# Kernel tuning notes

Hardware: AMD Instinct MI355X
Metric: run time of the kernel (lower is better)

The kernel has to match this reference:

```python
import jax, jax.numpy as jnp
import numpy as np

NPOINT = 1024
NSAMPLE = 32
RADIUS = 0.2


def index_points2(points, idx):
    # points: (B,N,D), idx: (B,S) -> (B,S,D)
    return jnp.take_along_axis(points, idx[..., None], axis=1)


def index_points3(points, idx):
    # points: (B,N,D), idx: (B,S,K) -> (B,S,K,D)
    B, S, K = idx.shape
    flat = jnp.take_along_axis(points, idx.reshape(B, S * K)[..., None], axis=1)
    return flat.reshape(B, S, K, points.shape[-1])


def farthest_point_sampling(xyz, npoint):
    # xyz: (B,N,3) -> (B,npoint) int32 indices. First point deterministic (index 0).
    B, N, _ = xyz.shape
    first = jnp.zeros((B,), jnp.int32)
    chosen = jnp.zeros((B, npoint), jnp.int32).at[:, 0].set(first)
    first_xyz = index_points2(xyz, first[:, None])[:, 0, :]
    dist_min = jnp.sum((xyz - first_xyz[:, None, :]) ** 2, axis=-1)  # (B,N)

    def body(i, carry):
        chosen, dist_min = carry
        far = jnp.argmax(dist_min, axis=-1).astype(jnp.int32)  # (B,)
        far_xyz = index_points2(xyz, far[:, None])[:, 0, :]
        d = jnp.sum((xyz - far_xyz[:, None, :]) ** 2, axis=-1)
        return chosen.at[:, i].set(far), jnp.minimum(dist_min, d)

    chosen, _ = jax.lax.fori_loop(1, npoint, body, (chosen, dist_min))
    return chosen


def query_ball_point(radius, nsample, xyz, new_xyz):
    # (B,S,N) squared distances; out-of-ball -> inf; take nsample nearest (stable argsort).
    dist = jnp.sum((new_xyz[:, :, None, :] - xyz[:, None, :, :]) ** 2, axis=-1)
    dist_m = jnp.where(dist <= radius ** 2, dist, jnp.inf)
    return jnp.argsort(dist_m, axis=-1)[:, :, :nsample]


def mlp2(x, Wa, ba, Wb, bb, act2):
    h = jax.nn.relu(x @ Wa + ba)
    return act2(h @ Wb + bb)


def reference(xyz, features, W1, b1, W2, b2, W3, b3, W4, b4):
    fps_idx = farthest_point_sampling(xyz, NPOINT)          # (B,S)
    new_xyz = index_points2(xyz, fps_idx)                   # (B,S,3)
    group_idx = query_ball_point(RADIUS, NSAMPLE, xyz, new_xyz)  # (B,S,K)
    grouped_xyz = index_points3(xyz, group_idx)             # (B,S,K,3)
    grouped_xyz_norm = grouped_xyz - new_xyz[:, :, None, :]
    grouped_feats = index_points3(features, group_idx)      # (B,S,K,C)
    f_in = jnp.concatenate([grouped_xyz_norm, grouped_feats], axis=-1)
    f_prime = mlp2(f_in, W1, b1, W2, b2, jax.nn.relu)       # (B,S,K,H)
    f_mean = jnp.mean(f_prime, axis=2, keepdims=True)
    w_in = jnp.concatenate([grouped_xyz_norm, f_prime - f_mean], axis=-1)
    alpha = mlp2(w_in, W3, b3, W4, b4, jax.nn.sigmoid)      # (B,S,K,H)
    f_out = jnp.sum(alpha * f_prime, axis=2)                # (B,S,H)
    return new_xyz, f_out


def setup_inputs() -> dict:
    key = jax.random.key(0)
    ks = jax.random.split(key, 8)
    B, N, C, H = 16, 4096, 64, 128
    xyz = jax.random.uniform(ks[0], (B, N, 3), dtype=jnp.float32)
    features = jax.random.normal(ks[1], (B, N, C), dtype=jnp.float32)
    s = 0.1
    return {
        "xyz": xyz,
        "features": features,
        "W1": jax.random.normal(ks[2], (3 + C, H), dtype=jnp.float32) * s,
        "b1": jnp.zeros((H,), jnp.float32),
        "W2": jax.random.normal(ks[3], (H, H), dtype=jnp.float32) * s,
        "b2": jnp.zeros((H,), jnp.float32),
        "W3": jax.random.normal(ks[4], (3 + H, H), dtype=jnp.float32) * s,
        "b3": jnp.zeros((H,), jnp.float32),
        "W4": jax.random.normal(ks[5], (H, H), dtype=jnp.float32) * s,
        "b4": jnp.zeros((H,), jnp.float32),
    }
```

## Files before the change

### kernel.cpp

```cpp
#include <hip/hip_runtime.h>

typedef unsigned short u16;
typedef unsigned int   u32;
typedef unsigned long long u64;
typedef short s8v __attribute__((ext_vector_type(8)));
typedef float f4v __attribute__((ext_vector_type(4)));
typedef float f2v __attribute__((ext_vector_type(2)));

#define STRIDE 168
#define CAP 512
#define OFF_G1 0
#define OFF_G2 12288
#define OFF_G3 28672
#define OFF_G4 49152

__device__ __forceinline__ float bf2f(u16 u){ return __uint_as_float(((u32)u)<<16); }
__device__ __forceinline__ u16 f2bf(float f){
  u32 u = __float_as_uint(f);
  return (u16)((u + 0x7FFFu + ((u>>16)&1u)) >> 16);
}
__device__ __forceinline__ float sqd(float ax,float ay,float az,float bx,float by,float bz){
  float dx=ax-bx, dy=ay-by, dz=az-bz;
  return __fadd_rn(__fadd_rn(__fmul_rn(dx,dx),__fmul_rn(dy,dy)),__fmul_rn(dz,dz));
}

#define WMAX_STEP(v, CTRL) { \
  u32 _t = (u32)__builtin_amdgcn_update_dpp(0, (int)(v), CTRL, 0xf, 0xf, false); \
  (v) = (v) > _t ? (v) : _t; }
#define QMAX64(k, CTRL) { \
  u32 _lo=(u32)(k), _hi=(u32)((k)>>32); \
  u32 _plo=(u32)__builtin_amdgcn_update_dpp(0,(int)_lo,CTRL,0xf,0xf,true); \
  u32 _phi=(u32)__builtin_amdgcn_update_dpp(0,(int)_hi,CTRL,0xf,0xf,true); \
  u64 _o=((u64)_phi<<32)|_plo; (k) = (k)>_o ? (k) : _o; }

__global__ __launch_bounds__(256) void fps_kernel(const float* __restrict__ xyz,
                                                  float* __restrict__ newxyz){
  __shared__ __align__(16) float S[4096*3];
  __shared__ u64 red[2][4];
  const int b = blockIdx.x, tid = threadIdx.x;
  const int lane = tid & 63, wv = tid >> 6;
  const float* xb = xyz + (size_t)b*4096*3;
  #pragma unroll
  for(int j=0;j<12;j++) ((float4*)S)[j*256+tid] = ((const float4*)xb)[j*256+tid];
  __syncthreads();
  f2v X[8],Y[8],Z[8],DM[8];
  const float x0=S[0], y0=S[1], z0=S[2];
  {
    #pragma clang fp contract(off)
    const f2v fx2={x0,x0}, fy2={y0,y0}, fz2={z0,z0};
    #pragma unroll
    for(int k2=0;k2<8;k2++){
      int p0 = tid*16 + 2*k2;
      X[k2] = (f2v){S[p0*3],   S[p0*3+3]};
      Y[k2] = (f2v){S[p0*3+1], S[p0*3+4]};
      Z[k2] = (f2v){S[p0*3+2], S[p0*3+5]};
      f2v dx=X[k2]-fx2, dy=Y[k2]-fy2, dz=Z[k2]-fz2;
      DM[k2] = (dx*dx + dy*dy) + dz*dz;
    }
  }
  if(tid==0){
    size_t o=(size_t)b*1024*3;
    newxyz[o]=x0; newxyz[o+1]=y0; newxyz[o+2]=z0;
  }
  for(int i=1;i<1024;i++){
    float vm = DM[0][0]; int jm = 0;
    #pragma unroll
    for(int j=1;j<16;j++){
      float dj = DM[j>>1][j&1];
      bool g = dj > vm; vm = g ? dj : vm; jm = g ? j : jm;
    }
    u32 w = __float_as_uint(vm);
    WMAX_STEP(w, 0x111); WMAX_STEP(w, 0x112); WMAX_STEP(w, 0x114);
    WMAX_STEP(w, 0x118); WMAX_STEP(w, 0x142); WMAX_STEP(w, 0x143);
    u32 wm = (u32)__builtin_amdgcn_readlane((int)w, 63);
    u64 msk = __ballot(__float_as_uint(vm) == wm);
    int ldr = __ffsll((unsigned long long)msk) - 1;
    int pj  = __builtin_amdgcn_readlane(jm, ldr);
    int p   = (wv*64 + ldr)*16 + pj;
    if(lane==0) red[i&1][wv] = ((u64)wm<<32) | (u32)(~(u32)p);
    __syncthreads();
    u64 k = red[i&1][lane&3];
    QMAX64(k, 0xB1); QMAX64(k, 0x4E);
    int far = (int)(~(u32)k) & 4095;
    float fx=S[far*3], fy=S[far*3+1], fz=S[far*3+2];
    if(tid==0){
      size_t o=((size_t)b*1024+i)*3;
      newxyz[o]=fx; newxyz[o+1]=fy; newxyz[o+2]=fz;
    }
    {
      #pragma clang fp contract(off)
      const f2v fx2={fx,fx}, fy2={fy,fy}, fz2={fz,fz};
      #pragma unroll
      for(int k2=0;k2<8;k2++){
        f2v dx=X[k2]-fx2, dy=Y[k2]-fy2, dz=Z[k2]-fz2;
        f2v s = (dx*dx + dy*dy) + dz*dz;
        DM[k2] = __builtin_elementwise_min(DM[k2], s);
      }
    }
  }
}

__global__ __launch_bounds__(256) void swz_kernel(const float* __restrict__ W1,const float* __restrict__ W2,
                                                  const float* __restrict__ W3,const float* __restrict__ W4,
                                                  u16* __restrict__ wsw){
  int T = blockIdx.x*256 + threadIdx.x;
  const float* W; int rel, base, kind;
  if(T < 1536){ rel=T;      base=OFF_G1; W=W1; kind=0; }
  else if(T < 3584){ rel=T-1536; base=OFF_G2; W=W2; kind=1; }
  else if(T < 6144){ rel=T-3584; base=OFF_G3; W=W3; kind=0; }
  else         { rel=T-6144; base=OFF_G4; W=W4; kind=1; }
  int chunk=rel>>6, lane=rel&63, c=chunk>>3, t=chunk&7, quad=lane>>4, l15=lane&15;
  u16 v[8];
  #pragma unroll
  for(int j=0;j<8;j++){
    int kp = c*32 + quad*8 + j, n = t*16 + l15;
    int src = (kind==0) ? (kp<3 ? kp : (kp>=32 ? kp-29 : -1)) : kp;
    v[j] = (src<0) ? (u16)0 : f2bf(W[src*128 + n]);
  }
  int4 o;
  o.x=(int)((u32)v[0]|((u32)v[1]<<16)); o.y=(int)((u32)v[2]|((u32)v[3]<<16));
  o.z=(int)((u32)v[4]|((u32)v[5]<<16)); o.w=(int)((u32)v[6]|((u32)v[7]<<16));
  *(int4*)&wsw[base + rel*8] = o;
}

__device__ __forceinline__ void zero_C(f4v C[2][8]){
  #pragma unroll
  for(int mt=0;mt<2;mt++)
    #pragma unroll
    for(int t=0;t<8;t++) C[mt][t] = (f4v){0.f,0.f,0.f,0.f};
}
__device__ __forceinline__ void load_bias(const float* bsrc,int l15,float bb[8]){
  #pragma unroll
  for(int t=0;t<8;t++) bb[t]=bsrc[t*16+l15];
}
template<int KC>
__device__ __forceinline__ void run_gemm(const u16* A, const u16* BW,
                                         int lane,int l15,int quad, f4v C[2][8]){
  s8v af[2][KC];
  #pragma unroll
  for(int mt=0;mt<2;mt++)
    #pragma unroll
    for(int c=0;c<KC;c++)
      af[mt][c] = *(const s8v*)&A[(mt*16+l15)*STRIDE + c*32 + quad*8];
  #pragma unroll
  for(int t=0;t<8;t++){
    #pragma unroll
    for(int c=0;c<KC;c++){
      s8v bw = *(const s8v*)&BW[((c*8+t)*64 + lane)*8];
      C[0][t] = __builtin_amdgcn_mfma_f32_16x16x32_bf16(af[0][c],bw,C[0][t],0,0,0);
      C[1][t] = __builtin_amdgcn_mfma_f32_16x16x32_bf16(af[1][c],bw,C[1][t],0,0,0);
    }
  }
}
__device__ __forceinline__ void store_act(u16* A,int l15,int quad,f4v C[2][8],const float bb[8]){
  #pragma unroll
  for(int mt=0;mt<2;mt++)
    #pragma unroll
    for(int t=0;t<8;t++)
      #pragma unroll
      for(int r=0;r<4;r++){
        float v = fmaxf(C[mt][t][r]+bb[t], 0.f);
        A[(mt*16+quad*4+r)*STRIDE + t*16 + l15] = f2bf(v);
      }
}
__device__ __forceinline__ void write_xyz_chunk0(u16* A,int lane,float xn,float yn,float zn){
  if(lane<32){
    u16* row=&A[lane*STRIDE];
    row[0]=f2bf(xn); row[1]=f2bf(yn); row[2]=f2bf(zn); row[3]=0;
    #pragma unroll
    for(int q=0;q<7;q++) *(u64*)&row[4+q*4] = 0ull;
  }
}

__global__ __launch_bounds__(256,2) void mlp_kernel(const float* __restrict__ xyz,
    const float* __restrict__ feats, const u16* __restrict__ wsw,
    const float* __restrict__ b1,const float* __restrict__ b2,const float* __restrict__ b3,const float* __restrict__ b4,
    const float* __restrict__ newxyz, float* __restrict__ fout){
  __shared__ __align__(16) u16 Abuf[4][32*STRIDE];
  __shared__ u64 Bcand[4][CAP];
  __shared__ int selbuf[4][32];
  const int tid=threadIdx.x, wv=tid>>6, lane=tid&63, quad=lane>>4, l15=lane&15;
  const int widx = blockIdx.x*4 + wv, b = widx>>10;
  u16* A = Abuf[wv];
  const float* xb = xyz + (size_t)b*4096*3;
  const float cx=newxyz[widx*3], cy=newxyz[widx*3+1], cz=newxyz[widx*3+2];

  {
    u64* Bc = Bcand[wv];
    int* sel = selbuf[wv];
    const u64 lt = (1ull<<lane)-1ull;
    int base=0;
    for(int kk=0;kk<64;kk++){
      int p = kk*64 + lane;
      float d = sqd(cx,cy,cz, xb[p*3],xb[p*3+1],xb[p*3+2]);
      bool in = (d <= 0.04f);
      u64 m = __ballot(in);
      if(in){ int pos = base + __popcll(m&lt); if(pos<CAP) Bc[pos] = ((u64)__float_as_uint(d)<<32)|(u32)p; }
      base += __popcll(m);
    }
    int cnt = base>CAP ? CAP : base;
    if(cnt > 32){
      for(int c=lane; c<cnt; c+=64){
        u64 key = Bc[c]; int r=0;
        for(int t2=0;t2<cnt;t2++) r += (Bc[t2] < key) ? 1 : 0;
        if(r < 32) sel[r] = (int)(u32)key;
      }
    } else {
      for(int c=lane; c<cnt; c+=64) sel[c] = (int)(u32)Bc[c];
      int need = 32 - cnt, b2 = 0;
      for(int kk=0; kk<64 && b2<need; kk++){
        int p = kk*64 + lane;
        float d = sqd(cx,cy,cz, xb[p*3],xb[p*3+1],xb[p*3+2]);
        bool o = !(d <= 0.04f);
        u64 m = __ballot(o);
        if(o){ int pos = b2 + __popcll(m&lt); if(pos<need) sel[cnt+pos] = p; }
        b2 += __popcll(m);
      }
    }
  }
  const int* sel = selbuf[wv];
  const int gi_f = sel[lane>>1] & 4095;
  const int gi_x = sel[lane & 31] & 4095;

  {
    int r2=lane>>1, h=lane&1;
    const float* fs = feats + ((size_t)b*4096 + gi_f)*64 + h*32;
    u16* fd = &A[r2*STRIDE + 32 + h*32];
    #pragma unroll
    for(int j=0;j<8;j++){
      float4 v4 = ((const float4*)fs)[j];
      u64 pk4 = (u64)f2bf(v4.x) | ((u64)f2bf(v4.y)<<16)
              | ((u64)f2bf(v4.z)<<32) | ((u64)f2bf(v4.w)<<48);
      *(u64*)&fd[j*4] = pk4;
    }
  }
  float xn=0.f,yn=0.f,zn=0.f;
  if(lane<32){
    const float* xp = xb + (size_t)gi_x*3;
    xn = xp[0]-cx; yn = xp[1]-cy; zn = xp[2]-cz;
  }
  write_xyz_chunk0(A,lane,xn,yn,zn);
  __syncthreads();

  f4v C[2][8]; float bb[8];
  zero_C(C); load_bias(b1,l15,bb);
  run_gemm<3>(A, wsw+OFF_G1, lane,l15,quad, C);
  store_act(A,l15,quad,C,bb);
  __syncthreads();
  zero_C(C); load_bias(b2,l15,bb);
  run_gemm<4>(A, wsw+OFF_G2, lane,l15,quad, C);
  float fp[2][8][4]; float mean[8];
  #pragma unroll
  for(int t=0;t<8;t++){
    float s=0.f;
    #pragma unroll
    for(int mt=0;mt<2;mt++)
      #pragma unroll
      for(int r=0;r<4;r++){
        float v = fmaxf(C[mt][t][r]+bb[t], 0.f);
        fp[mt][t][r]=v; s+=v;
      }
    s += __shfl_xor(s,16); s += __shfl_xor(s,32);
    mean[t] = s*0.03125f;
  }
  #pragma unroll
  for(int mt=0;mt<2;mt++)
    #pragma unroll
    for(int t=0;t<8;t++)
      #pragma unroll
      for(int r=0;r<4;r++)
        A[(mt*16+quad*4+r)*STRIDE + 32 + t*16 + l15] = f2bf(fp[mt][t][r]-mean[t]);
  write_xyz_chunk0(A,lane,xn,yn,zn);
  __syncthreads();
  zero_C(C); load_bias(b3,l15,bb);
  run_gemm<5>(A, wsw+OFF_G3, lane,l15,quad, C);
  store_act(A,l15,quad,C,bb);
  __syncthreads();
  zero_C(C); load_bias(b4,l15,bb);
  run_gemm<4>(A, wsw+OFF_G4, lane,l15,quad, C);
  float* fo = fout + (size_t)widx*128;
  #pragma unroll
  for(int t=0;t<8;t++){
    float part=0.f;
    #pragma unroll
    for(int mt=0;mt<2;mt++)
      #pragma unroll
      for(int r=0;r<4;r++){
        float pre = C[mt][t][r]+bb[t];
        float a = 1.f/(1.f+__expf(-pre));
        part += a*fp[mt][t][r];
      }
    part += __shfl_xor(part,16); part += __shfl_xor(part,32);
    if(quad==0) fo[t*16+l15] = part;
  }
}

extern "C" void kernel_launch(void* const* d_in, const int* in_sizes, int n_in,
                              void* d_out, int out_size, void* d_ws, size_t ws_size,
                              hipStream_t stream){
  (void)in_sizes; (void)n_in; (void)out_size; (void)ws_size;
  const float* xyz   = (const float*)d_in[0];
  const float* feats = (const float*)d_in[1];
  const float* W1 = (const float*)d_in[2]; const float* b1 = (const float*)d_in[3];
  const float* W2 = (const float*)d_in[4]; const float* b2 = (const float*)d_in[5];
  const float* W3 = (const float*)d_in[6]; const float* b3 = (const float*)d_in[7];
  const float* W4 = (const float*)d_in[8]; const float* b4 = (const float*)d_in[9];
  float* out = (float*)d_out;
  float* newxyz = out;
  float* fout   = out + 16*1024*3;
  u16* wsw = (u16*)d_ws;

  hipLaunchKernelGGL(swz_kernel, dim3(32),   dim3(256), 0, stream, W1,W2,W3,W4, wsw);
  hipLaunchKernelGGL(fps_kernel, dim3(16),   dim3(256), 0, stream, xyz, newxyz);
  hipLaunchKernelGGL(mlp_kernel, dim3(4096), dim3(256), 0, stream,
                     xyz, feats, wsw, b1,b2,b3,b4, newxyz, fout);
}
```

Before: 1.024 ms.

## Tree-reduce FPS argmax, stage sampled points in LDS, raise MLP occupancy

The per-thread argmax in FPS becomes a packed-max tree followed by an equality bitmask and ffs, which shortens the serial compare chain inside the 1023-iteration loop. Sampled centroids are buffered in LDS and written out once with coalesced float4 stores, replacing per-iteration global stores. Separately, the MLP kernel's candidate buffer capacity is halved and its launch bound is raised to 3 blocks per CU to increase occupancy. The smaller capacity risks overflow if a ball holds more candidates than the buffer allows, and the tighter register budget may cause spills.

```diff
diff --git a/kernel.cpp b/kernel.cpp
--- a/kernel.cpp
+++ b/kernel.cpp
@@ -8,7 +8,7 @@
 typedef float f2v __attribute__((ext_vector_type(2)));
 
 #define STRIDE 168
-#define CAP 512
+#define CAP 256
 #define OFF_G1 0
 #define OFF_G2 12288
 #define OFF_G3 28672
@@ -36,6 +36,7 @@
 __global__ __launch_bounds__(256) void fps_kernel(const float* __restrict__ xyz,
                                                   float* __restrict__ newxyz){
   __shared__ __align__(16) float S[4096*3];
+  __shared__ __align__(16) float R[1024*3];
   __shared__ u64 red[2][4];
   const int b = blockIdx.x, tid = threadIdx.x;
   const int lane = tid & 63, wv = tid >> 6;
@@ -58,17 +59,18 @@
       DM[k2] = (dx*dx + dy*dy) + dz*dz;
     }
   }
-  if(tid==0){
-    size_t o=(size_t)b*1024*3;
-    newxyz[o]=x0; newxyz[o+1]=y0; newxyz[o+2]=z0;
-  }
+  if(tid==0){ R[0]=x0; R[1]=y0; R[2]=z0; }
   for(int i=1;i<1024;i++){
-    float vm = DM[0][0]; int jm = 0;
-    #pragma unroll
-    for(int j=1;j<16;j++){
-      float dj = DM[j>>1][j&1];
-      bool g = dj > vm; vm = g ? dj : vm; jm = g ? j : jm;
-    }
+    f2v a = __builtin_elementwise_max(__builtin_elementwise_max(DM[0],DM[1]),
+                                      __builtin_elementwise_max(DM[2],DM[3]));
+    f2v c = __builtin_elementwise_max(__builtin_elementwise_max(DM[4],DM[5]),
+                                      __builtin_elementwise_max(DM[6],DM[7]));
+    f2v mm = __builtin_elementwise_max(a,c);
+    float vm = fmaxf(mm[0], mm[1]);
+    u32 m16 = 0;
+    #pragma unroll
+    for(int j=0;j<16;j++) m16 |= (DM[j>>1][j&1]==vm) ? (1u<<j) : 0u;
+    int jm = __ffs(m16)-1;
     u32 w = __float_as_uint(vm);
     WMAX_STEP(w, 0x111); WMAX_STEP(w, 0x112); WMAX_STEP(w, 0x114);
     WMAX_STEP(w, 0x118); WMAX_STEP(w, 0x142); WMAX_STEP(w, 0x143);
@@ -83,21 +85,22 @@
     QMAX64(k, 0xB1); QMAX64(k, 0x4E);
     int far = (int)(~(u32)k) & 4095;
     float fx=S[far*3], fy=S[far*3+1], fz=S[far*3+2];
-    if(tid==0){
-      size_t o=((size_t)b*1024+i)*3;
-      newxyz[o]=fx; newxyz[o+1]=fy; newxyz[o+2]=fz;
-    }
+    if(tid==0){ R[i*3]=fx; R[i*3+1]=fy; R[i*3+2]=fz; }
     {
       #pragma clang fp contract(off)
       const f2v fx2={fx,fx}, fy2={fy,fy}, fz2={fz,fz};
       #pragma unroll
-      for(int k2=0;k2<8;k2++){
-        f2v dx=X[k2]-fx2, dy=Y[k2]-fy2, dz=Z[k2]-fz2;
+      for(int k2c=0;k2c<8;k2c++){
+        f2v dx=X[k2c]-fx2, dy=Y[k2c]-fy2, dz=Z[k2c]-fz2;
         f2v s = (dx*dx + dy*dy) + dz*dz;
-        DM[k2] = __builtin_elementwise_min(DM[k2], s);
-      }
-    }
-  }
+        DM[k2c] = __builtin_elementwise_min(DM[k2c], s);
+      }
+    }
+  }
+  __syncthreads();
+  float* nb = newxyz + (size_t)b*3072;
+  #pragma unroll
+  for(int j=0;j<3;j++) ((float4*)nb)[j*256+tid] = ((const float4*)R)[j*256+tid];
 }
 
 __global__ __launch_bounds__(256) void swz_kernel(const float* __restrict__ W1,const float* __restrict__ W2,
@@ -172,7 +175,7 @@
   }
 }
 
-__global__ __launch_bounds__(256,2) void mlp_kernel(const float* __restrict__ xyz,
+__global__ __launch_bounds__(256,3) void mlp_kernel(const float* __restrict__ xyz,
     const float* __restrict__ feats, const u16* __restrict__ wsw,
     const float* __restrict__ b1,const float* __restrict__ b2,const float* __restrict__ b3,const float* __restrict__ b4,
     const float* __restrict__ newxyz, float* __restrict__ fout){
```

Result: no change. 1.010 ms (-1.3%).
